# Performance work log

Hardware: AMD Instinct MI355X
Metric: run time of the kernel (lower is better)

The kernel has to match this reference:

```python
import jax, jax.numpy as jnp
import numpy as np

N_IN, N_LAT, LEN_T, N_SHIFT = 128, 21, 51, 50
N_HID, BATCH = 4, 2048


def identity_init(n_rows, n_cols):
    A = np.zeros((n_rows, n_cols), np.float32)
    if n_rows >= n_cols:
        k = n_rows - n_cols + 1
        for c in range(n_cols):
            A[c:c + k, c] = 1.0 / k
    else:
        k = n_cols - n_rows + 1
        for r in range(n_rows):
            A[r, r:r + k] = 1.0 / k
    return jnp.asarray(A)


def setup_inputs() -> dict:
    key = jax.random.key(0)
    ks = jax.random.split(key, 8)
    s = 0.05
    return {
        'inputs': jax.random.normal(ks[0], (BATCH, LEN_T, N_IN), dtype=jnp.float32),
        'enc_W': jax.random.normal(ks[1], (N_HID, N_IN, N_IN), dtype=jnp.float32) * s,
        'enc_b': jnp.zeros((N_HID, N_IN), jnp.float32),
        'enc_Wout': jax.random.normal(ks[2], (N_IN, N_IN), dtype=jnp.float32) * s,
        'enc_bout': jnp.zeros((N_IN,), jnp.float32),
        'dec_W': jax.random.normal(ks[3], (N_HID, N_IN, N_IN), dtype=jnp.float32) * s,
        'dec_b': jnp.zeros((N_HID, N_IN), jnp.float32),
        'dec_Wout': jax.random.normal(ks[4], (N_IN, N_IN), dtype=jnp.float32) * s,
        'dec_bout': jnp.zeros((N_IN,), jnp.float32),
        'W_enc_inner': identity_init(N_IN, N_LAT),
        'L': jnp.eye(N_LAT, dtype=jnp.float32),
        'W_dec_inner': identity_init(N_LAT, N_IN),
    }


def res_block(x, Ws, bs, Wout, bout):
    # DenseResBlock: ReLU hidden dense stack + linear output + identity skip
    h = x
    for i in range(Ws.shape[0]):
        h = jax.nn.relu(h @ Ws[i] + bs[i])
    return h @ Wout + bout + x


def reference(inputs, enc_W, enc_b, enc_Wout, enc_bout,
              dec_W, dec_b, dec_Wout, dec_bout,
              W_enc_inner, L, W_dec_inner):
    B = inputs.shape[0]
    len_pred = LEN_T - N_SHIFT  # = 1

    # ---- autoencoder branch (all timesteps flattened into rows) ----
    auto_in = inputs.reshape(-1, N_IN)                       # [B*T, n_in]
    part_enc = res_block(auto_in, enc_W, enc_b, enc_Wout, enc_bout)
    full_enc = part_enc @ W_enc_inner                        # [B*T, n_lat]
    part_dec = full_enc @ W_dec_inner                        # [B*T, n_in]
    autoencoder_output = res_block(part_dec, dec_W, dec_b, dec_Wout, dec_bout)
    autoencoder_output = autoencoder_output.reshape(B, LEN_T, N_IN)
    outer_auto_output = res_block(part_enc, dec_W, dec_b, dec_Wout, dec_bout)
    outer_auto_output = outer_auto_output.reshape(B, LEN_T, N_IN)

    # ---- prediction branch: recurrent application of Koopman operator L ----
    pred_in = inputs[:, :len_pred, :].reshape(-1, N_IN)      # [B*len_pred, n_in]
    cur = res_block(pred_in, enc_W, enc_b, enc_Wout, enc_bout) @ W_enc_inner

    def step(cur_enc, _):
        adv = cur_enc @ L                                    # [B*len_pred, n_lat]
        dec = res_block(adv @ W_dec_inner, dec_W, dec_b, dec_Wout, dec_bout)
        return adv, dec

    _, preds = jax.lax.scan(step, cur, None, length=N_SHIFT)  # [S, B*lp, n_in]
    preds = preds.reshape(N_SHIFT, B, len_pred, N_IN)
    predictions = preds.transpose(1, 0, 2, 3).reshape(B, N_SHIFT * len_pred, N_IN)

    return autoencoder_output, outer_auto_output, predictions
```

## Files before the change

### kernel.cpp

```cpp
#include <hip/hip_runtime.h>
#include <stdint.h>


typedef _Float16 h8 __attribute__((ext_vector_type(8)));
typedef float    f4 __attribute__((ext_vector_type(4)));

#define ROWS_AUTO 104448
#define NTILE     3264

#define WT_ENCW      0
#define WT_ENCWOUT   (4*16384)
#define WT_DECW      (5*16384)
#define WT_DECWOUT   (9*16384)
#define WT_COMB      (10*16384)

#define MFULL_OFF_B 0x60000
#define ACH_OFF_B   0x200000

#define LDS_BYTES 43520

__device__ __forceinline__ f4 mfma16(h8 a, h8 b, f4 c) {
  return __builtin_amdgcn_mfma_f32_16x16x32_f16(a, b, c, 0, 0, 0);
}
__device__ __forceinline__ h8 cvt8(f4 a, f4 b) {
  h8 r;
  r[0]=(_Float16)a[0]; r[1]=(_Float16)a[1]; r[2]=(_Float16)a[2]; r[3]=(_Float16)a[3];
  r[4]=(_Float16)b[0]; r[5]=(_Float16)b[1]; r[6]=(_Float16)b[2]; r[7]=(_Float16)b[3];
  return r;
}
__device__ __forceinline__ int hsw(int rl, int c) { return rl*256 + ((c ^ (rl & 7)) << 4); }
__device__ __forceinline__ int tsw(int r, int q) { return 24576 + r*512 + ((q ^ ((r & 7) << 2)) << 4); }

__device__ __forceinline__ void loadW(h8 B[8], const _Float16* gW, int nbase, int r15, int hi) {
#pragma unroll
  for (int nt = 0; nt < 2; ++nt)
#pragma unroll
    for (int ks = 0; ks < 4; ++ks)
      B[nt*4+ks] = *(const h8*)(gW + (size_t)(nbase + nt*16 + r15)*128 + ks*32 + hi*8);
}

__device__ __forceinline__ void mmF(const char* sm, int hb, const h8 B[8],
                                    f4 acc[2][2], int r15, int hi) {
#pragma unroll
  for (int rt = 0; rt < 2; ++rt)
#pragma unroll
    for (int nt = 0; nt < 2; ++nt) acc[rt][nt] = (f4){0.f,0.f,0.f,0.f};
#pragma unroll
  for (int ks = 0; ks < 4; ++ks) {
    int c = ks*4 + hi;
    h8 a0 = *(const h8*)(sm + hb + hsw(r15, c));
    h8 a1 = *(const h8*)(sm + hb + hsw(16 + r15, c));
    acc[0][0] = mfma16(a0, B[ks],   acc[0][0]);
    acc[0][1] = mfma16(a0, B[4+ks], acc[0][1]);
    acc[1][0] = mfma16(a1, B[ks],   acc[1][0]);
    acc[1][1] = mfma16(a1, B[4+ks], acc[1][1]);
  }
}

__device__ __forceinline__ void hwrite(char* sm, int hb, int wbase, const f4 acc[2][2],
                                       const float* bl, int bo, int r15, int hi) {
#pragma unroll
  for (int nt = 0; nt < 2; ++nt) {
    int n = wbase + nt*16 + r15;
    float bv = bl[bo + n];
#pragma unroll
    for (int rt = 0; rt < 2; ++rt)
#pragma unroll
      for (int d = 0; d < 4; ++d) {
        int r = rt*16 + hi*4 + d;
        float v = fmaxf(acc[rt][nt][d] + bv, 0.f);
        *(_Float16*)(sm + hb + hsw(r, n >> 3) + (n & 7)*2) = (_Float16)v;
      }
  }
}

template<bool NT>
__device__ __forceinline__ void store_rows(const char* sm, float* gbase, int rstride, int tid) {
  int rr = tid >> 3, qb = tid & 7;
#pragma unroll
  for (int i = 0; i < 4; ++i) {
    int q = i*8 + qb;
    f4 v = *(const f4*)(sm + tsw(rr, q));
    if (NT) __builtin_nontemporal_store(v, (f4*)(gbase + (size_t)rr*rstride + q*4));
    else    *(f4*)(gbase + (size_t)rr*rstride + q*4) = v;
  }
}

#define LAYER(BW, BO) do {                                   \
    mmF(sm, cur*8192, BW, acc, r15, hi);                     \
    hwrite(sm, (cur^1)*8192, wbase, acc, bl, BO, r15, hi);   \
    __syncthreads(); cur ^= 1;                               \
  } while (0)


__global__ __launch_bounds__(512) void k_prep(
    const float* __restrict__ encW, const float* __restrict__ encWout,
    const float* __restrict__ decW, const float* __restrict__ decWout,
    const float* __restrict__ L,
    _Float16* __restrict__ wt, float* __restrict__ ach) {
  __shared__ float chA[441], chB[441];
  int m = blockIdx.y, tid = threadIdx.x;
  if (m == 10) {
    if (blockIdx.x != 0) return;
    if (tid < 441) chA[tid] = L[tid];
    __syncthreads();
    for (int s = 0; s < 50; ++s) {
      if (tid < 441) ach[s*441 + tid] = chA[tid];
      if (s == 49) break;
      if (tid < 441) {
        int i = tid / 21, j = tid % 21; float a = 0.f;
        for (int k = 0; k < 21; ++k) a += chA[i*21 + k] * L[k*21 + j];
        chB[tid] = a;
      }
      __syncthreads();
      if (tid < 441) chA[tid] = chB[tid];
      __syncthreads();
    }
    return;
  }
  int idx = blockIdx.x*512 + tid;
  if (idx >= 16384) return;
  const float* src; _Float16* dst;
  if (m < 4)       { src = encW + m*16384;     dst = wt + WT_ENCW + m*16384; }
  else if (m == 4) { src = encWout;            dst = wt + WT_ENCWOUT; }
  else if (m < 9)  { src = decW + (m-5)*16384; dst = wt + WT_DECW + (m-5)*16384; }
  else             { src = decWout;            dst = wt + WT_DECWOUT; }
  int n = idx >> 7, k = idx & 127;
  dst[idx] = (_Float16)src[k*128 + n];
}

__global__ __launch_bounds__(512) void k_aux(
    const float* __restrict__ ach, const float* __restrict__ wencI,
    const float* __restrict__ wdecI,
    _Float16* __restrict__ mfull, _Float16* __restrict__ wt) {
  __shared__ float T1[2688];
  __shared__ float sa[441];
  int s = blockIdx.x, t = threadIdx.x;
  if (s < 50) {
    if (t < 441) sa[t] = ach[s*441 + t];
    __syncthreads();
    for (int idx = t; idx < 2688; idx += 512) {
      int k = idx / 21, j = idx % 21;
      float a = 0.f;
      for (int u = 0; u < 21; ++u) a += wencI[k*21 + u] * sa[u*21 + j];
      T1[idx] = a;
    }
  } else {
    for (int idx = t; idx < 2688; idx += 512) T1[idx] = wencI[idx];
  }
  __syncthreads();
  _Float16* dst = (s < 50) ? (mfull + (size_t)s*16384) : (wt + WT_COMB);
  for (int idx = t; idx < 16384; idx += 512) {
    int n = idx >> 7, k = idx & 127;
    float a = 0.f;
    for (int j = 0; j < 21; ++j) a += T1[k*21 + j] * wdecI[j*128 + n];
    dst[idx] = (_Float16)a;
  }
}


__global__ __launch_bounds__(256, 2) void k_enc(
    const float* __restrict__ x, const _Float16* __restrict__ wt,
    const float* __restrict__ enc_b, const float* __restrict__ enc_bout,
    float* __restrict__ out1, float* __restrict__ out2) {
  __shared__ char sm[LDS_BYTES];
  float* bl = (float*)(sm + 40960);
  int tid = threadIdx.x, lane = tid & 63;
  int r15 = lane & 15, hi = lane >> 4;
  int wbase = (tid >> 6) * 32;
  h8 B0[8], B1[8], B2[8], B3[8], B4[8], B5[8];
  loadW(B0, wt + WT_ENCW,           wbase, r15, hi);
  loadW(B1, wt + WT_ENCW + 16384,   wbase, r15, hi);
  loadW(B2, wt + WT_ENCW + 2*16384, wbase, r15, hi);
  loadW(B3, wt + WT_ENCW + 3*16384, wbase, r15, hi);
  loadW(B4, wt + WT_ENCWOUT,        wbase, r15, hi);
  loadW(B5, wt + WT_COMB,           wbase, r15, hi);
  bl[tid] = enc_b[tid]; bl[256 + tid] = enc_b[256 + tid];
  if (tid < 128) bl[512 + tid] = enc_bout[tid];
  f4 acc[2][2];

  for (int t = blockIdx.x; t < NTILE; t += gridDim.x) {
    size_t rowbase = (size_t)t * 32;
#pragma unroll
    for (int i = 0; i < 2; ++i) {
      int idx = i*256 + tid, rl = idx >> 4, c = idx & 15;
      const float* s = x + (rowbase + rl)*128 + c*8;
      f4 v0 = *(const f4*)s, v1 = *(const f4*)(s + 4);
      h8 hv = cvt8(v0, v1);
      int off = hsw(rl, c);
      *(h8*)(sm + off) = hv;
      *(h8*)(sm + 16384 + off) = hv;
    }
    __syncthreads();
    int cur = 0;
    LAYER(B0, 0); LAYER(B1, 128); LAYER(B2, 256); LAYER(B3, 384);
    mmF(sm, cur*8192, B4, acc, r15, hi);
#pragma unroll
    for (int nt = 0; nt < 2; ++nt) {
      int n = wbase + nt*16 + r15;
      float bv = bl[512 + n];
#pragma unroll
      for (int rt = 0; rt < 2; ++rt)
#pragma unroll
        for (int d = 0; d < 4; ++d) {
          int r = rt*16 + hi*4 + d;
          float sk = (float)*(const _Float16*)(sm + 16384 + hsw(r, n >> 3) + (n & 7)*2);
          float v = acc[rt][nt][d] + bv + sk;
          *(_Float16*)(sm + (cur^1)*8192 + hsw(r, n >> 3) + (n & 7)*2) = (_Float16)v;
          *(float*)(sm + tsw(r, n >> 2) + (n & 3)*4) = v;
        }
    }
    __syncthreads();
    store_rows<false>(sm, out2 + rowbase*128, 128, tid);
    cur ^= 1;
    mmF(sm, cur*8192, B5, acc, r15, hi);
    __syncthreads();
#pragma unroll
    for (int nt = 0; nt < 2; ++nt) {
      int n = wbase + nt*16 + r15;
#pragma unroll
      for (int rt = 0; rt < 2; ++rt)
#pragma unroll
        for (int d = 0; d < 4; ++d) {
          int r = rt*16 + hi*4 + d;
          *(float*)(sm + tsw(r, n >> 2) + (n & 3)*4) = acc[rt][nt][d];
        }
    }
    __syncthreads();
    store_rows<false>(sm, out1 + rowbase*128, 128, tid);
    __syncthreads();
  }
}


__global__ __launch_bounds__(256, 2) void k_dec(
    const _Float16* __restrict__ wt,
    const float* __restrict__ dec_b, const float* __restrict__ dec_bout,
    float* __restrict__ out1, float* __restrict__ out2) {
  __shared__ char sm[LDS_BYTES];
  float* bl = (float*)(sm + 40960);
  int tid = threadIdx.x, lane = tid & 63;
  int r15 = lane & 15, hi = lane >> 4;
  int wbase = (tid >> 6) * 32;
  h8 B0[8], B1[8], B2[8], B3[8], B4[8];
  loadW(B0, wt + WT_DECW,           wbase, r15, hi);
  loadW(B1, wt + WT_DECW + 16384,   wbase, r15, hi);
  loadW(B2, wt + WT_DECW + 2*16384, wbase, r15, hi);
  loadW(B3, wt + WT_DECW + 3*16384, wbase, r15, hi);
  loadW(B4, wt + WT_DECWOUT,        wbase, r15, hi);
  bl[tid] = dec_b[tid]; bl[256 + tid] = dec_b[256 + tid];
  if (tid < 128) bl[512 + tid] = dec_bout[tid];
  f4 acc[2][2];

  for (int t = blockIdx.x; t < 2*NTILE; t += gridDim.x) {
    int rt0 = (t >= NTILE) ? t - NTILE : t;
    float* io = (t >= NTILE) ? out1 : out2;
    float* p = io + (size_t)rt0 * 32 * 128;
#pragma unroll
    for (int i = 0; i < 2; ++i) {
      int idx = i*256 + tid, rl = idx >> 4, c = idx & 15;
      const float* s = p + rl*128 + c*8;
      f4 v0 = *(const f4*)s, v1 = *(const f4*)(s + 4);
      h8 hv = cvt8(v0, v1);
      int off = hsw(rl, c);
      *(h8*)(sm + off) = hv;
      *(h8*)(sm + 16384 + off) = hv;
    }
    __syncthreads();
    int cur = 0;
    LAYER(B0, 0); LAYER(B1, 128); LAYER(B2, 256); LAYER(B3, 384);
    mmF(sm, cur*8192, B4, acc, r15, hi);
#pragma unroll
    for (int nt = 0; nt < 2; ++nt) {
      int n = wbase + nt*16 + r15;
      float bv = bl[512 + n];
#pragma unroll
      for (int rt = 0; rt < 2; ++rt)
#pragma unroll
        for (int d = 0; d < 4; ++d) {
          int r = rt*16 + hi*4 + d;
          float sk = (float)*(const _Float16*)(sm + 16384 + hsw(r, n >> 3) + (n & 7)*2);
          float v = acc[rt][nt][d] + bv + sk;
          *(float*)(sm + tsw(r, n >> 2) + (n & 3)*4) = v;
        }
    }
    __syncthreads();
    store_rows<true>(sm, p, 128, tid);
    __syncthreads();
  }
}


__global__ __launch_bounds__(256, 2) void k_pred(
    const float* __restrict__ pe_src, const _Float16* __restrict__ wt,
    const _Float16* __restrict__ mfull,
    const float* __restrict__ dec_b, const float* __restrict__ dec_bout,
    float* __restrict__ out3) {
  __shared__ char sm[LDS_BYTES];
  float* bl = (float*)(sm + 40960);
  int tid = threadIdx.x, lane = tid & 63;
  int r15 = lane & 15, hi = lane >> 4;
  int wbase = (tid >> 6) * 32;
  h8 B0[8], B1[8], B2[8], B3[8], B4[8];
  loadW(B0, wt + WT_DECW,           wbase, r15, hi);
  loadW(B1, wt + WT_DECW + 16384,   wbase, r15, hi);
  loadW(B2, wt + WT_DECW + 2*16384, wbase, r15, hi);
  loadW(B3, wt + WT_DECW + 3*16384, wbase, r15, hi);
  loadW(B4, wt + WT_DECWOUT,        wbase, r15, hi);
  bl[tid] = dec_b[tid]; bl[256 + tid] = dec_b[256 + tid];
  if (tid < 128) bl[512 + tid] = dec_bout[tid];
  f4 acc[2][2];

  for (int u = blockIdx.x; u < 50*64; u += gridDim.x) {
    int s = u >> 6, rtile = u & 63;
    size_t bbase = (size_t)rtile * 32;
    h8 Bm[8];
    loadW(Bm, mfull + (size_t)s*16384, wbase, r15, hi);
#pragma unroll
    for (int i = 0; i < 2; ++i) {
      int idx = i*256 + tid, rl = idx >> 4, c = idx & 15;
      const float* src = pe_src + (bbase + rl)*51*128 + c*8;
      f4 v0 = *(const f4*)src, v1 = *(const f4*)(src + 4);
      *(h8*)(sm + hsw(rl, c)) = cvt8(v0, v1);
    }
    __syncthreads();
    mmF(sm, 0, Bm, acc, r15, hi);
#pragma unroll
    for (int nt = 0; nt < 2; ++nt) {
      int n = wbase + nt*16 + r15;
#pragma unroll
      for (int rt = 0; rt < 2; ++rt)
#pragma unroll
        for (int d = 0; d < 4; ++d) {
          int r = rt*16 + hi*4 + d;
          _Float16 hv = (_Float16)acc[rt][nt][d];
          *(_Float16*)(sm + 8192 + hsw(r, n >> 3) + (n & 7)*2) = hv;
          *(_Float16*)(sm + 16384 + hsw(r, n >> 3) + (n & 7)*2) = hv;
        }
    }
    __syncthreads();
    int cur = 1;
    LAYER(B0, 0); LAYER(B1, 128); LAYER(B2, 256); LAYER(B3, 384);
    mmF(sm, cur*8192, B4, acc, r15, hi);
#pragma unroll
    for (int nt = 0; nt < 2; ++nt) {
      int n = wbase + nt*16 + r15;
      float bv = bl[512 + n];
#pragma unroll
      for (int rt = 0; rt < 2; ++rt)
#pragma unroll
        for (int d = 0; d < 4; ++d) {
          int r = rt*16 + hi*4 + d;
          float sk = (float)*(const _Float16*)(sm + 16384 + hsw(r, n >> 3) + (n & 7)*2);
          float v = acc[rt][nt][d] + bv + sk;
          *(float*)(sm + tsw(r, n >> 2) + (n & 3)*4) = v;
        }
    }
    __syncthreads();
    store_rows<true>(sm, out3 + (bbase*50 + s)*128, 50*128, tid);
    __syncthreads();
  }
}


extern "C" void kernel_launch(void* const* d_in, const int* in_sizes, int n_in,
                              void* d_out, int out_size, void* d_ws, size_t ws_size,
                              hipStream_t stream) {
  const float* x        = (const float*)d_in[0];
  const float* encW     = (const float*)d_in[1];
  const float* enc_b    = (const float*)d_in[2];
  const float* encWout  = (const float*)d_in[3];
  const float* enc_bout = (const float*)d_in[4];
  const float* decW     = (const float*)d_in[5];
  const float* dec_b    = (const float*)d_in[6];
  const float* decWout  = (const float*)d_in[7];
  const float* dec_bout = (const float*)d_in[8];
  const float* wencI    = (const float*)d_in[9];
  const float* L        = (const float*)d_in[10];
  const float* wdecI    = (const float*)d_in[11];

  char* ws = (char*)d_ws;
  _Float16* wt    = (_Float16*)ws;
  _Float16* mfull = (_Float16*)(ws + MFULL_OFF_B);
  float*    ach   = (float*)(ws + ACH_OFF_B);

  float* out1 = (float*)d_out;
  float* out2 = out1 + (size_t)ROWS_AUTO*128;
  float* out3 = out2 + (size_t)ROWS_AUTO*128;

  hipLaunchKernelGGL(k_prep, dim3(32, 11), dim3(512), 0, stream,
                     encW, encWout, decW, decWout, L, wt, ach);
  hipLaunchKernelGGL(k_aux, dim3(51), dim3(512), 0, stream,
                     ach, wencI, wdecI, mfull, wt);
  hipLaunchKernelGGL(k_enc, dim3(512), dim3(256), 0, stream,
                     x, wt, enc_b, enc_bout, out1, out2);
  hipLaunchKernelGGL(k_pred, dim3(512), dim3(256), 0, stream,
                     out2, wt, mfull, dec_b, dec_bout, out3);
  hipLaunchKernelGGL(k_dec, dim3(512), dim3(256), 0, stream,
                     wt, dec_b, dec_bout, out1, out2);
}
```

Before: 244.0 us.

## Stage encoder intermediates in fp16 workspace and use 64-row tiles

The encoder now writes its part_enc and combined-projection intermediates as swizzled fp16 tiles to workspace buffers instead of fp32 into the output arrays. The decoder and prediction kernels read those compact tiles directly, which removes a float-to-half conversion pass and halves intermediate traffic. Encoder and decoder tiles grow from 32 to 64 rows to reuse register-resident weights over more MFMAs. The prediction kernel loads its input tile once and loops over 5 shift steps per block, with a 640-block grid. The trade-off is higher register and LDS use per block, plus an extra workspace round trip where outputs were previously written in place.

```diff
diff --git a/kernel.cpp b/kernel.cpp
--- a/kernel.cpp
+++ b/kernel.cpp
@@ -6,7 +6,7 @@
 typedef float    f4 __attribute__((ext_vector_type(4)));
 
 #define ROWS_AUTO 104448
-#define NTILE     3264
+#define NT64      1632
 
 #define WT_ENCW      0
 #define WT_ENCWOUT   (4*16384)
@@ -16,8 +16,20 @@
 
 #define MFULL_OFF_B 0x60000
 #define ACH_OFF_B   0x200000
-
-#define LDS_BYTES 43520
+#define PE_OFF_B    0x220000
+#define PD_OFF_B    0x1C00000
+
+#define H0 0
+#define H1 16384
+#define H2 32768
+#define LDSE 51712
+#define HP 0
+#define P0 8192
+#define P1 16384
+#define P2 24576
+#define LDSP 35328
+
+#define hsw(rl, c) ((rl)*256 + ((((c)) ^ ((rl) & 7)) << 4))
 
 __device__ __forceinline__ f4 mfma16(h8 a, h8 b, f4 c) {
   return __builtin_amdgcn_mfma_f32_16x16x32_f16(a, b, c, 0, 0, 0);
@@ -28,9 +40,6 @@
   r[4]=(_Float16)b[0]; r[5]=(_Float16)b[1]; r[6]=(_Float16)b[2]; r[7]=(_Float16)b[3];
   return r;
 }
-__device__ __forceinline__ int hsw(int rl, int c) { return rl*256 + ((c ^ (rl & 7)) << 4); }
-__device__ __forceinline__ int tsw(int r, int q) { return 24576 + r*512 + ((q ^ ((r & 7) << 2)) << 4); }
-
 __device__ __forceinline__ void loadW(h8 B[8], const _Float16* gW, int nbase, int r15, int hi) {
 #pragma unroll
   for (int nt = 0; nt < 2; ++nt)
@@ -39,12 +48,27 @@
       B[nt*4+ks] = *(const h8*)(gW + (size_t)(nbase + nt*16 + r15)*128 + ks*32 + hi*8);
 }
 
-__device__ __forceinline__ void mmF(const char* sm, int hb, const h8 B[8],
-                                    f4 acc[2][2], int r15, int hi) {
-#pragma unroll
-  for (int rt = 0; rt < 2; ++rt)
-#pragma unroll
-    for (int nt = 0; nt < 2; ++nt) acc[rt][nt] = (f4){0.f,0.f,0.f,0.f};
+__device__ __forceinline__ void mmF4(const char* sm, int hb, const h8 B[8],
+                                     f4 acc[4][2], int r15, int hi) {
+#pragma unroll
+  for (int rt = 0; rt < 4; ++rt) { acc[rt][0] = (f4){0,0,0,0}; acc[rt][1] = (f4){0,0,0,0}; }
+#pragma unroll
+  for (int ks = 0; ks < 4; ++ks) {
+    int c = ks*4 + hi;
+    h8 a[4];
+#pragma unroll
+    for (int rt = 0; rt < 4; ++rt) a[rt] = *(const h8*)(sm + hb + hsw(rt*16 + r15, c));
+#pragma unroll
+    for (int rt = 0; rt < 4; ++rt) {
+      acc[rt][0] = mfma16(a[rt], B[ks],   acc[rt][0]);
+      acc[rt][1] = mfma16(a[rt], B[4+ks], acc[rt][1]);
+    }
+  }
+}
+__device__ __forceinline__ void mmF2(const char* sm, int hb, const h8 B[8],
+                                     f4 acc[2][2], int r15, int hi) {
+#pragma unroll
+  for (int rt = 0; rt < 2; ++rt) { acc[rt][0] = (f4){0,0,0,0}; acc[rt][1] = (f4){0,0,0,0}; }
 #pragma unroll
   for (int ks = 0; ks < 4; ++ks) {
     int c = ks*4 + hi;
@@ -57,14 +81,13 @@
   }
 }
 
-__device__ __forceinline__ void hwrite(char* sm, int hb, int wbase, const f4 acc[2][2],
-                                       const float* bl, int bo, int r15, int hi) {
+__device__ __forceinline__ void hw4(char* sm, int hb, int wbase, const f4 acc[4][2],
+                                    const float* bl, int bo, int r15, int hi) {
 #pragma unroll
   for (int nt = 0; nt < 2; ++nt) {
-    int n = wbase + nt*16 + r15;
-    float bv = bl[bo + n];
-#pragma unroll
-    for (int rt = 0; rt < 2; ++rt)
+    int n = wbase + nt*16 + r15; float bv = bl[bo + n];
+#pragma unroll
+    for (int rt = 0; rt < 4; ++rt)
 #pragma unroll
       for (int d = 0; d < 4; ++d) {
         int r = rt*16 + hi*4 + d;
@@ -73,24 +96,21 @@
       }
   }
 }
-
-template<bool NT>
-__device__ __forceinline__ void store_rows(const char* sm, float* gbase, int rstride, int tid) {
-  int rr = tid >> 3, qb = tid & 7;
-#pragma unroll
-  for (int i = 0; i < 4; ++i) {
-    int q = i*8 + qb;
-    f4 v = *(const f4*)(sm + tsw(rr, q));
-    if (NT) __builtin_nontemporal_store(v, (f4*)(gbase + (size_t)rr*rstride + q*4));
-    else    *(f4*)(gbase + (size_t)rr*rstride + q*4) = v;
-  }
-}
-
-#define LAYER(BW, BO) do {                                   \
-    mmF(sm, cur*8192, BW, acc, r15, hi);                     \
-    hwrite(sm, (cur^1)*8192, wbase, acc, bl, BO, r15, hi);   \
-    __syncthreads(); cur ^= 1;                               \
-  } while (0)
+__device__ __forceinline__ void hw2(char* sm, int hb, int wbase, const f4 acc[2][2],
+                                    const float* bl, int bo, int r15, int hi) {
+#pragma unroll
+  for (int nt = 0; nt < 2; ++nt) {
+    int n = wbase + nt*16 + r15; float bv = bl[bo + n];
+#pragma unroll
+    for (int rt = 0; rt < 2; ++rt)
+#pragma unroll
+      for (int d = 0; d < 4; ++d) {
+        int r = rt*16 + hi*4 + d;
+        float v = fmaxf(acc[rt][nt][d] + bv, 0.f);
+        *(_Float16*)(sm + hb + hsw(r, n >> 3) + (n & 7)*2) = (_Float16)v;
+      }
+  }
+}
 
 
 __global__ __launch_bounds__(512) void k_prep(
@@ -162,83 +182,89 @@
 __global__ __launch_bounds__(256, 2) void k_enc(
     const float* __restrict__ x, const _Float16* __restrict__ wt,
     const float* __restrict__ enc_b, const float* __restrict__ enc_bout,
-    float* __restrict__ out1, float* __restrict__ out2) {
-  __shared__ char sm[LDS_BYTES];
-  float* bl = (float*)(sm + 40960);
+    _Float16* __restrict__ pe_ws, _Float16* __restrict__ pd_ws) {
+  __shared__ char sm[LDSE];
+  float* bl = (float*)(sm + 49152);
   int tid = threadIdx.x, lane = tid & 63;
   int r15 = lane & 15, hi = lane >> 4;
   int wbase = (tid >> 6) * 32;
-  h8 B0[8], B1[8], B2[8], B3[8], B4[8], B5[8];
-  loadW(B0, wt + WT_ENCW,           wbase, r15, hi);
+  h8 B0[8], B1[8], B2[8], B3[8], B4[8];
   loadW(B1, wt + WT_ENCW + 16384,   wbase, r15, hi);
   loadW(B2, wt + WT_ENCW + 2*16384, wbase, r15, hi);
   loadW(B3, wt + WT_ENCW + 3*16384, wbase, r15, hi);
   loadW(B4, wt + WT_ENCWOUT,        wbase, r15, hi);
-  loadW(B5, wt + WT_COMB,           wbase, r15, hi);
   bl[tid] = enc_b[tid]; bl[256 + tid] = enc_b[256 + tid];
   if (tid < 128) bl[512 + tid] = enc_bout[tid];
-  f4 acc[2][2];
-
-  for (int t = blockIdx.x; t < NTILE; t += gridDim.x) {
-    size_t rowbase = (size_t)t * 32;
-#pragma unroll
-    for (int i = 0; i < 2; ++i) {
+  f4 acc[4][2];
+
+  for (int t = blockIdx.x; t < NT64; t += gridDim.x) {
+    loadW(B0, wt + WT_ENCW, wbase, r15, hi);
+    size_t rb = (size_t)t * 64;
+#pragma unroll
+    for (int i = 0; i < 4; ++i) {
       int idx = i*256 + tid, rl = idx >> 4, c = idx & 15;
-      const float* s = x + (rowbase + rl)*128 + c*8;
+      const float* s = x + (rb + rl)*128 + c*8;
       f4 v0 = *(const f4*)s, v1 = *(const f4*)(s + 4);
-      h8 hv = cvt8(v0, v1);
-      int off = hsw(rl, c);
-      *(h8*)(sm + off) = hv;
-      *(h8*)(sm + 16384 + off) = hv;
-    }
-    __syncthreads();
-    int cur = 0;
-    LAYER(B0, 0); LAYER(B1, 128); LAYER(B2, 256); LAYER(B3, 384);
-    mmF(sm, cur*8192, B4, acc, r15, hi);
+      *(h8*)(sm + H0 + hsw(rl, c)) = cvt8(v0, v1);
+    }
+    __syncthreads();
+    mmF4(sm, H0, B0, acc, r15, hi);
+    loadW(B0, wt + WT_COMB, wbase, r15, hi);
+    hw4(sm, H1, wbase, acc, bl, 0,   r15, hi); __syncthreads();
+    mmF4(sm, H1, B1, acc, r15, hi); hw4(sm, H2, wbase, acc, bl, 128, r15, hi); __syncthreads();
+    mmF4(sm, H2, B2, acc, r15, hi); hw4(sm, H1, wbase, acc, bl, 256, r15, hi); __syncthreads();
+    mmF4(sm, H1, B3, acc, r15, hi); hw4(sm, H2, wbase, acc, bl, 384, r15, hi); __syncthreads();
+    mmF4(sm, H2, B4, acc, r15, hi);
+#pragma unroll
+    for (int nt = 0; nt < 2; ++nt) {
+      int n = wbase + nt*16 + r15; float bv = bl[512 + n];
+#pragma unroll
+      for (int rt = 0; rt < 4; ++rt)
+#pragma unroll
+        for (int d = 0; d < 4; ++d) {
+          int r = rt*16 + hi*4 + d;
+          float sk = (float)*(const _Float16*)(sm + H0 + hsw(r, n >> 3) + (n & 7)*2);
+          float v = acc[rt][nt][d] + bv + sk;
+          *(_Float16*)(sm + H1 + hsw(r, n >> 3) + (n & 7)*2) = (_Float16)v;
+        }
+    }
+    __syncthreads();
+    {
+      char* g = (char*)(pe_ws) + (size_t)t*16384;
+#pragma unroll
+      for (int i = 0; i < 4; ++i) { int off = (i*256 + tid)*16;
+        *(f4*)(g + off) = *(const f4*)(sm + H1 + off); }
+    }
+    mmF4(sm, H1, B0, acc, r15, hi);
 #pragma unroll
     for (int nt = 0; nt < 2; ++nt) {
       int n = wbase + nt*16 + r15;
-      float bv = bl[512 + n];
-#pragma unroll
-      for (int rt = 0; rt < 2; ++rt)
+#pragma unroll
+      for (int rt = 0; rt < 4; ++rt)
 #pragma unroll
         for (int d = 0; d < 4; ++d) {
           int r = rt*16 + hi*4 + d;
-          float sk = (float)*(const _Float16*)(sm + 16384 + hsw(r, n >> 3) + (n & 7)*2);
-          float v = acc[rt][nt][d] + bv + sk;
-          *(_Float16*)(sm + (cur^1)*8192 + hsw(r, n >> 3) + (n & 7)*2) = (_Float16)v;
-          *(float*)(sm + tsw(r, n >> 2) + (n & 3)*4) = v;
+          *(_Float16*)(sm + H2 + hsw(r, n >> 3) + (n & 7)*2) = (_Float16)acc[rt][nt][d];
         }
     }
     __syncthreads();
-    store_rows<false>(sm, out2 + rowbase*128, 128, tid);
-    cur ^= 1;
-    mmF(sm, cur*8192, B5, acc, r15, hi);
-    __syncthreads();
-#pragma unroll
-    for (int nt = 0; nt < 2; ++nt) {
-      int n = wbase + nt*16 + r15;
-#pragma unroll
-      for (int rt = 0; rt < 2; ++rt)
-#pragma unroll
-        for (int d = 0; d < 4; ++d) {
-          int r = rt*16 + hi*4 + d;
-          *(float*)(sm + tsw(r, n >> 2) + (n & 3)*4) = acc[rt][nt][d];
-        }
-    }
-    __syncthreads();
-    store_rows<false>(sm, out1 + rowbase*128, 128, tid);
-    __syncthreads();
+    {
+      char* g = (char*)(pd_ws) + (size_t)t*16384;
+#pragma unroll
+      for (int i = 0; i < 4; ++i) { int off = (i*256 + tid)*16;
+        *(f4*)(g + off) = *(const f4*)(sm + H2 + off); }
+    }
   }
 }
 
 
 __global__ __launch_bounds__(256, 2) void k_dec(
-    const _Float16* __restrict__ wt,
+    const _Float16* __restrict__ wt, const _Float16* __restrict__ pe_ws,
+    const _Float16* __restrict__ pd_ws,
     const float* __restrict__ dec_b, const float* __restrict__ dec_bout,
     float* __restrict__ out1, float* __restrict__ out2) {
-  __shared__ char sm[LDS_BYTES];
-  float* bl = (float*)(sm + 40960);
+  __shared__ char sm[LDSE];
+  float* bl = (float*)(sm + 49152);
   int tid = threadIdx.x, lane = tid & 63;
   int r15 = lane & 15, hi = lane >> 4;
   int wbase = (tid >> 6) * 32;
@@ -250,58 +276,63 @@
   loadW(B4, wt + WT_DECWOUT,        wbase, r15, hi);
   bl[tid] = dec_b[tid]; bl[256 + tid] = dec_b[256 + tid];
   if (tid < 128) bl[512 + tid] = dec_bout[tid];
-  f4 acc[2][2];
-
-  for (int t = blockIdx.x; t < 2*NTILE; t += gridDim.x) {
-    int rt0 = (t >= NTILE) ? t - NTILE : t;
-    float* io = (t >= NTILE) ? out1 : out2;
-    float* p = io + (size_t)rt0 * 32 * 128;
-#pragma unroll
-    for (int i = 0; i < 2; ++i) {
-      int idx = i*256 + tid, rl = idx >> 4, c = idx & 15;
-      const float* s = p + rl*128 + c*8;
-      f4 v0 = *(const f4*)s, v1 = *(const f4*)(s + 4);
-      h8 hv = cvt8(v0, v1);
-      int off = hsw(rl, c);
-      *(h8*)(sm + off) = hv;
-      *(h8*)(sm + 16384 + off) = hv;
-    }
-    __syncthreads();
-    int cur = 0;
-    LAYER(B0, 0); LAYER(B1, 128); LAYER(B2, 256); LAYER(B3, 384);
-    mmF(sm, cur*8192, B4, acc, r15, hi);
+  f4 acc[4][2];
+
+  for (int u = blockIdx.x; u < 2*NT64; u += gridDim.x) {
+    int t = (u >= NT64) ? u - NT64 : u;
+    const char* src = (const char*)((u >= NT64) ? pd_ws : pe_ws) + (size_t)t*16384;
+    float* dst = ((u >= NT64) ? out1 : out2) + (size_t)t*64*128;
+#pragma unroll
+    for (int i = 0; i < 4; ++i) {
+      int off = (i*256 + tid)*16;
+      *(f4*)(sm + H0 + off) = *(const f4*)(src + off);
+    }
+    __syncthreads();
+    mmF4(sm, H0, B0, acc, r15, hi); hw4(sm, H1, wbase, acc, bl, 0,   r15, hi); __syncthreads();
+    mmF4(sm, H1, B1, acc, r15, hi); hw4(sm, H2, wbase, acc, bl, 128, r15, hi); __syncthreads();
+    mmF4(sm, H2, B2, acc, r15, hi); hw4(sm, H1, wbase, acc, bl, 256, r15, hi); __syncthreads();
+    mmF4(sm, H1, B3, acc, r15, hi); hw4(sm, H2, wbase, acc, bl, 384, r15, hi); __syncthreads();
+    mmF4(sm, H2, B4, acc, r15, hi);
+    __syncthreads();
 #pragma unroll
     for (int nt = 0; nt < 2; ++nt) {
-      int n = wbase + nt*16 + r15;
-      float bv = bl[512 + n];
-#pragma unroll
-      for (int rt = 0; rt < 2; ++rt)
+      int n = wbase + nt*16 + r15; float bv = bl[512 + n];
+      int q = n >> 2;
+#pragma unroll
+      for (int rt = 0; rt < 4; ++rt)
 #pragma unroll
         for (int d = 0; d < 4; ++d) {
           int r = rt*16 + hi*4 + d;
-          float sk = (float)*(const _Float16*)(sm + 16384 + hsw(r, n >> 3) + (n & 7)*2);
+          float sk = (float)*(const _Float16*)(sm + H0 + hsw(r, n >> 3) + (n & 7)*2);
           float v = acc[rt][nt][d] + bv + sk;
-          *(float*)(sm + tsw(r, n >> 2) + (n & 3)*4) = v;
+          *(float*)(sm + H1 + r*512 + ((q ^ ((r & 7) << 2)) << 4) + (n & 3)*4) = v;
         }
     }
     __syncthreads();
-    store_rows<true>(sm, p, 128, tid);
-    __syncthreads();
+    {
+      int rr = tid >> 2, qb = (tid & 3)*8;
+#pragma unroll
+      for (int i = 0; i < 8; ++i) {
+        int q = qb + i;
+        f4 v = *(const f4*)(sm + H1 + rr*512 + ((q ^ ((rr & 7) << 2)) << 4));
+        __builtin_nontemporal_store(v, (f4*)(dst + (size_t)rr*128 + q*4));
+      }
+    }
   }
 }
 
 
 __global__ __launch_bounds__(256, 2) void k_pred(
-    const float* __restrict__ pe_src, const _Float16* __restrict__ wt,
+    const _Float16* __restrict__ pe_ws, const _Float16* __restrict__ wt,
     const _Float16* __restrict__ mfull,
     const float* __restrict__ dec_b, const float* __restrict__ dec_bout,
     float* __restrict__ out3) {
-  __shared__ char sm[LDS_BYTES];
-  float* bl = (float*)(sm + 40960);
+  __shared__ char sm[LDSP];
+  float* bl = (float*)(sm + 32768);
   int tid = threadIdx.x, lane = tid & 63;
   int r15 = lane & 15, hi = lane >> 4;
   int wbase = (tid >> 6) * 32;
-  h8 B0[8], B1[8], B2[8], B3[8], B4[8];
+  h8 B0[8], B1[8], B2[8], B3[8], B4[8], Bm[8];
   loadW(B0, wt + WT_DECW,           wbase, r15, hi);
   loadW(B1, wt + WT_DECW + 16384,   wbase, r15, hi);
   loadW(B2, wt + WT_DECW + 2*16384, wbase, r15, hi);
@@ -311,20 +342,21 @@
   if (tid < 128) bl[512 + tid] = dec_bout[tid];
   f4 acc[2][2];
 
-  for (int u = blockIdx.x; u < 50*64; u += gridDim.x) {
-    int s = u >> 6, rtile = u & 63;
-    size_t bbase = (size_t)rtile * 32;
-    h8 Bm[8];
+  int rtile = blockIdx.x / 10, chunk = blockIdx.x % 10;
+#pragma unroll
+  for (int i = 0; i < 2; ++i) {
+    int idx = i*256 + tid, rl = idx >> 4, c = idx & 15;
+    int rg = rtile*32 + rl;
+    int r  = rg * 51;
+    const char* sp = (const char*)pe_ws + (size_t)(r >> 6)*16384
+                   + (r & 63)*256 + ((c ^ ((r & 63) & 7)) << 4);
+    *(f4*)(sm + HP + hsw(rl, c)) = *(const f4*)sp;
+  }
+  __syncthreads();
+
+  for (int s = chunk*5; s < chunk*5 + 5; ++s) {
     loadW(Bm, mfull + (size_t)s*16384, wbase, r15, hi);
-#pragma unroll
-    for (int i = 0; i < 2; ++i) {
-      int idx = i*256 + tid, rl = idx >> 4, c = idx & 15;
-      const float* src = pe_src + (bbase + rl)*51*128 + c*8;
-      f4 v0 = *(const f4*)src, v1 = *(const f4*)(src + 4);
-      *(h8*)(sm + hsw(rl, c)) = cvt8(v0, v1);
-    }
-    __syncthreads();
-    mmF(sm, 0, Bm, acc, r15, hi);
+    mmF2(sm, HP, Bm, acc, r15, hi);
 #pragma unroll
     for (int nt = 0; nt < 2; ++nt) {
       int n = wbase + nt*16 + r15;
@@ -333,31 +365,41 @@
 #pragma unroll
         for (int d = 0; d < 4; ++d) {
           int r = rt*16 + hi*4 + d;
-          _Float16 hv = (_Float16)acc[rt][nt][d];
-          *(_Float16*)(sm + 8192 + hsw(r, n >> 3) + (n & 7)*2) = hv;
-          *(_Float16*)(sm + 16384 + hsw(r, n >> 3) + (n & 7)*2) = hv;
+          *(_Float16*)(sm + P0 + hsw(r, n >> 3) + (n & 7)*2) = (_Float16)acc[rt][nt][d];
         }
     }
     __syncthreads();
-    int cur = 1;
-    LAYER(B0, 0); LAYER(B1, 128); LAYER(B2, 256); LAYER(B3, 384);
-    mmF(sm, cur*8192, B4, acc, r15, hi);
+    mmF2(sm, P0, B0, acc, r15, hi); hw2(sm, P1, wbase, acc, bl, 0,   r15, hi); __syncthreads();
+    mmF2(sm, P1, B1, acc, r15, hi); hw2(sm, P2, wbase, acc, bl, 128, r15, hi); __syncthreads();
+    mmF2(sm, P2, B2, acc, r15, hi); hw2(sm, P1, wbase, acc, bl, 256, r15, hi); __syncthreads();
+    mmF2(sm, P1, B3, acc, r15, hi); hw2(sm, P2, wbase, acc, bl, 384, r15, hi); __syncthreads();
+    mmF2(sm, P2, B4, acc, r15, hi);
+    __syncthreads();
 #pragma unroll
     for (int nt = 0; nt < 2; ++nt) {
-      int n = wbase + nt*16 + r15;
-      float bv = bl[512 + n];
+      int n = wbase + nt*16 + r15; float bv = bl[512 + n];
+      int q = n >> 2;
 #pragma unroll
       for (int rt = 0; rt < 2; ++rt)
 #pragma unroll
         for (int d = 0; d < 4; ++d) {
           int r = rt*16 + hi*4 + d;
-          float sk = (float)*(const _Float16*)(sm + 16384 + hsw(r, n >> 3) + (n & 7)*2);
+          float sk = (float)*(const _Float16*)(sm + P0 + hsw(r, n >> 3) + (n & 7)*2);
           float v = acc[rt][nt][d] + bv + sk;
-          *(float*)(sm + tsw(r, n >> 2) + (n & 3)*4) = v;
+          *(float*)(sm + P1 + r*512 + ((q ^ ((r & 7) << 2)) << 4) + (n & 3)*4) = v;
         }
     }
     __syncthreads();
-    store_rows<true>(sm, out3 + (bbase*50 + s)*128, 50*128, tid);
+    {
+      int rr = tid >> 3, qb = (tid & 7)*4;
+      size_t b = (size_t)(rtile*32 + rr);
+#pragma unroll
+      for (int i = 0; i < 4; ++i) {
+        int q = qb + i;
+        f4 v = *(const f4*)(sm + P1 + rr*512 + ((q ^ ((rr & 7) << 2)) << 4));
+        __builtin_nontemporal_store(v, (f4*)(out3 + (b*50 + s)*128 + q*4));
+      }
+    }
     __syncthreads();
   }
 }
@@ -383,6 +425,8 @@
   _Float16* wt    = (_Float16*)ws;
   _Float16* mfull = (_Float16*)(ws + MFULL_OFF_B);
   float*    ach   = (float*)(ws + ACH_OFF_B);
+  _Float16* pe_ws = (_Float16*)(ws + PE_OFF_B);
+  _Float16* pd_ws = (_Float16*)(ws + PD_OFF_B);
 
   float* out1 = (float*)d_out;
   float* out2 = out1 + (size_t)ROWS_AUTO*128;
@@ -393,9 +437,9 @@
   hipLaunchKernelGGL(k_aux, dim3(51), dim3(512), 0, stream,
                      ach, wencI, wdecI, mfull, wt);
   hipLaunchKernelGGL(k_enc, dim3(512), dim3(256), 0, stream,
-                     x, wt, enc_b, enc_bout, out1, out2);
-  hipLaunchKernelGGL(k_pred, dim3(512), dim3(256), 0, stream,
-                     out2, wt, mfull, dec_b, dec_bout, out3);
+                     x, wt, enc_b, enc_bout, pe_ws, pd_ws);
+  hipLaunchKernelGGL(k_pred, dim3(640), dim3(256), 0, stream,
+                     pe_ws, wt, mfull, dec_b, dec_bout, out3);
   hipLaunchKernelGGL(k_dec, dim3(512), dim3(256), 0, stream,
-                     wt, dec_b, dec_bout, out1, out2);
-}
+                     wt, pe_ws, pd_ws, dec_b, dec_bout, out1, out2);
+}
```

Result: slower. 467.6 us (+91.6%).
